# Kernel optimization log

Measured on AMD Instinct MI355X. Metric: run time of the kernel, lower is better.

## Reference

```python
import jax, jax.numpy as jnp
import numpy as np

# --- fixed OpenCV filter kernels ---
# cv2.getGaussianKernel(3, 1): exp(-(i-1)^2/2), normalized -> [0.27407, 0.45186, 0.27407]
_g = np.exp(-((np.arange(3) - 1.0) ** 2) / 2.0)
GAUSS_1D = (_g / _g.sum()).astype(np.float32)
# cv2 Sobel/Laplacian ksize=9 separable parts (unnormalized, as cv2.Laplacian uses):
#   smoothing = binomial row C(8,k); second derivative = C(6,k) conv [1,-2,1]
SMOOTH_9 = np.array([1, 8, 28, 56, 70, 56, 28, 8, 1], dtype=np.float32)
D2_9 = np.array([1, 4, 4, -4, -10, -4, 4, 4, 1], dtype=np.float32)


def _depthwise_conv(x, k2d):
    """Depthwise 2D correlation with BORDER_REFLECT_101 padding (cv2 default).

    x: [N,H,W,C] float, k2d: [kh,kw] float (symmetric, so corr == conv)."""
    C = x.shape[-1]
    rh, rw = k2d.shape[0] // 2, k2d.shape[1] // 2
    # jnp 'reflect' == OpenCV BORDER_REFLECT_101 (edge pixel not duplicated)
    xp = jnp.pad(x, ((0, 0), (rh, rh), (rw, rw), (0, 0)), mode='reflect')
    k = jnp.broadcast_to(k2d[:, :, None, None], (k2d.shape[0], k2d.shape[1], 1, C))
    return jax.lax.conv_general_dilated(
        xp, k, window_strides=(1, 1), padding='VALID',
        dimension_numbers=('NHWC', 'HWIO', 'NHWC'),
        feature_group_count=C)


def setup_inputs() -> dict:
    key = jax.random.key(0)
    # uint8-range image batch, as the original layer feeds uint8 data to OpenCV
    x = jax.random.uniform(key, (32, 512, 512, 3), dtype=jnp.float32) * 255.0
    return {"x": x}


def reference(x) -> jnp.ndarray:
    g = jnp.asarray(GAUSS_1D)
    blur = _depthwise_conv(x, jnp.outer(g, g))  # GaussianBlur(ksize=3, sigma=1)
    lap_k = jnp.asarray(np.outer(SMOOTH_9, D2_9) + np.outer(D2_9, SMOOTH_9))
    lap = _depthwise_conv(blur, lap_k) + 1.0  # delta = 1
    # CV_8UC1 destination depth -> saturate to [0, 255]
    return jnp.clip(lap, 0.0, 255.0)
```

## Files before the change

### kernel.cpp

```cpp
#include <hip/hip_runtime.h>


#define TH 32
#define TW 32
#define FW (TW*3)
#define BW (TW+8)
#define BF (BW*3)
#define BH (TH+8)
#define XHMAX (TH+10)
#define HIMG 512
#define WIMG 512
#define ROWF (WIMG*3)

#define SM_TOTAL 12480

__device__ __forceinline__ int reflect101(int i, int n) {
    i = (i < 0) ? -i : i;
    return (i >= n) ? (2 * n - 2 - i) : i;
}

__device__ __forceinline__ float4 fma4(float s, const float4& a, const float4& b) {
    return make_float4(fmaf(s, a.x, b.x), fmaf(s, a.y, b.y),
                       fmaf(s, a.z, b.z), fmaf(s, a.w, b.w));
}

__global__ __launch_bounds__(256, 3)
void log_fused(const float* __restrict__ x, float* __restrict__ out) {
    __shared__ __align__(16) float smem[SM_TOTAL];
    __shared__ int brow[BH][3];
    float* const blur  = smem;
    float* const hblur = smem + 4800;
    float* const t1    = smem + 4800;
    float* const t2    = smem + 8640;

    const int tid  = threadIdx.x;
    const int col0 = blockIdx.x * TW;
    const int row0 = blockIdx.y * TH;
    const int n    = blockIdx.z;

    const int R0    = max(0, row0 - 5);
    const int R1    = min(HIMG - 1, row0 + TH + 4);
    const int nrows = R1 - R0 + 1;

    if (tid < BH) {
        int gr = reflect101(row0 - 4 + tid, HIMG);
        brow[tid][0] = reflect101(gr - 1, HIMG) - R0;
        brow[tid][1] = gr - R0;
        brow[tid][2] = reflect101(gr + 1, HIMG) - R0;
    }

    const float G0 = 0.2740686190f, G1 = 0.4518627620f;

    if (tid < 240) {
        const int lc  = tid % BF;
        const int rg  = tid / BF;
        const int lcp = lc / 3;
        const int ch  = lc - 3 * lcp;
        const int gc  = reflect101(col0 - 4 + lcp, WIMG);
        const int xm  = reflect101(gc - 1, WIMG) * 3 + ch;
        const int x0  = gc * 3 + ch;
        const int xp  = reflect101(gc + 1, WIMG) * 3 + ch;
        const float* xr = x + ((size_t)n * HIMG + (size_t)(R0 + rg)) * ROWF;
        for (int r = rg; r < nrows; r += 2, xr += 2 * ROWF) {
            hblur[r * BF + lc] = G0 * (xr[xm] + xr[xp]) + G1 * xr[x0];
        }
    }
    __syncthreads();

    for (int e = tid; e < (BH * BF) / 4; e += 256) {
        int lr = e / (BF / 4);
        int qc = e - lr * (BF / 4);
        int lc = qc * 4;
        const float4 a = *(const float4*)&hblur[brow[lr][0] * BF + lc];
        const float4 b = *(const float4*)&hblur[brow[lr][1] * BF + lc];
        const float4 c = *(const float4*)&hblur[brow[lr][2] * BF + lc];
        float4 r;
        r.x = G0 * (a.x + c.x) + G1 * b.x;
        r.y = G0 * (a.y + c.y) + G1 * b.y;
        r.z = G0 * (a.z + c.z) + G1 * b.z;
        r.w = G0 * (a.w + c.w) + G1 * b.w;
        *(float4*)&blur[lr * BF + lc] = r;
    }
    __syncthreads();

    const float S9[9] = {1.f, 8.f, 28.f, 56.f, 70.f, 56.f, 28.f, 8.f, 1.f};
    const float D9[9] = {1.f, 4.f, 4.f, -4.f, -10.f, -4.f, 4.f, 4.f, 1.f};

    for (int g = tid; g < (TH / 2) * (BF / 4); g += 256) {
        int rg  = g / (BF / 4);
        int qc  = g - rg * (BF / 4);
        int lr0 = rg * 2;
        int lc  = qc * 4;
        float4 w[10];
        #pragma unroll
        for (int k = 0; k < 10; ++k)
            w[k] = *(const float4*)&blur[(lr0 + k) * BF + lc];
        float4 a1r0 = make_float4(0.f, 0.f, 0.f, 0.f), a2r0 = a1r0;
        float4 a1r1 = a1r0, a2r1 = a1r0;
        #pragma unroll
        for (int k = 0; k < 9; ++k) {
            a1r0 = fma4(S9[k], w[k],     a1r0);
            a2r0 = fma4(D9[k], w[k],     a2r0);
            a1r1 = fma4(S9[k], w[k + 1], a1r1);
            a2r1 = fma4(D9[k], w[k + 1], a2r1);
        }
        *(float4*)&t1[(lr0    ) * BF + lc] = a1r0;
        *(float4*)&t1[(lr0 + 1) * BF + lc] = a1r1;
        *(float4*)&t2[(lr0    ) * BF + lc] = a2r0;
        *(float4*)&t2[(lr0 + 1) * BF + lc] = a2r1;
    }
    __syncthreads();

    float* const outn = out + (size_t)n * HIMG * ROWF;
    for (int g = tid; g < TH * (FW / 8); g += 256) {
        int lr = g / (FW / 8);
        int qp = g - lr * (FW / 8);
        int lc = qp * 8;
        float w1[32], w2[32];
        #pragma unroll
        for (int q = 0; q < 8; ++q) {
            float4 v = *(const float4*)&t1[lr * BF + lc + 4 * q];
            w1[4*q+0] = v.x; w1[4*q+1] = v.y; w1[4*q+2] = v.z; w1[4*q+3] = v.w;
            float4 u = *(const float4*)&t2[lr * BF + lc + 4 * q];
            w2[4*q+0] = u.x; w2[4*q+1] = u.y; w2[4*q+2] = u.z; w2[4*q+3] = u.w;
        }
        float o[8];
        #pragma unroll
        for (int j = 0; j < 8; ++j) {
            float a = 1.0f;
            #pragma unroll
            for (int k = 0; k < 9; ++k) {
                a = fmaf(D9[k], w1[j + 3 * k], a);
                a = fmaf(S9[k], w2[j + 3 * k], a);
            }
            o[j] = fminf(fmaxf(a, 0.0f), 255.0f);
        }
        float* op = outn + (size_t)(row0 + lr) * ROWF + (size_t)(col0 * 3 + lc);
        *(float4*)&op[0] = make_float4(o[0], o[1], o[2], o[3]);
        *(float4*)&op[4] = make_float4(o[4], o[5], o[6], o[7]);
    }
}

extern "C" void kernel_launch(void* const* d_in, const int* in_sizes, int n_in,
                              void* d_out, int out_size, void* d_ws, size_t ws_size,
                              hipStream_t stream) {
    const float* x = (const float*)d_in[0];
    float* outp = (float*)d_out;
    const int nimg = in_sizes[0] / (HIMG * WIMG * 3);
    dim3 grid(WIMG / TW, HIMG / TH, nimg);
    log_fused<<<grid, dim3(256, 1, 1), 0, stream>>>(x, outp);
}
```

Before: 252.7 us.

## Halve tile height, vectorize interior horizontal blur, and shrink per-thread register windows

Tile height drops from 32 to 16 rows, shared memory shrinks, and launch bounds rise to 6 blocks per CU to raise occupancy. Interior column tiles load the input with float4 reads and compute the horizontal Gaussian from register shuffles, while edge tiles keep the reflected scalar path. The final horizontal pass now produces 4 outputs per thread from a 28-float streaming window instead of 8 outputs from 32-float arrays, which lowers register pressure. The cost is more halo overhead per output (8 halo rows per 16 instead of per 32), which means more redundant input reads and blur work.

```diff
diff --git a/kernel.cpp b/kernel.cpp
--- a/kernel.cpp
+++ b/kernel.cpp
@@ -1,18 +1,16 @@
 #include <hip/hip_runtime.h>
 
 
-#define TH 32
+#define TH 16
 #define TW 32
 #define FW (TW*3)
-#define BW (TW+8)
-#define BF (BW*3)
+#define BF ((TW+8)*3)
 #define BH (TH+8)
-#define XHMAX (TH+10)
 #define HIMG 512
 #define WIMG 512
 #define ROWF (WIMG*3)
 
-#define SM_TOTAL 12480
+#define SM_TOTAL 6720
 
 __device__ __forceinline__ int reflect101(int i, int n) {
     i = (i < 0) ? -i : i;
@@ -24,14 +22,13 @@
                        fmaf(s, a.z, b.z), fmaf(s, a.w, b.w));
 }
 
-__global__ __launch_bounds__(256, 3)
+__global__ __launch_bounds__(256, 6)
 void log_fused(const float* __restrict__ x, float* __restrict__ out) {
     __shared__ __align__(16) float smem[SM_TOTAL];
-    __shared__ int brow[BH][3];
-    float* const blur  = smem;
-    float* const hblur = smem + 4800;
-    float* const t1    = smem + 4800;
-    float* const t2    = smem + 8640;
+    float* const hblur = smem;
+    float* const t1    = smem;
+    float* const t2    = smem + TH * BF;
+    float* const blur  = smem + 2 * TH * BF;
 
     const int tid  = threadIdx.x;
     const int col0 = blockIdx.x * TW;
@@ -42,38 +39,57 @@
     const int R1    = min(HIMG - 1, row0 + TH + 4);
     const int nrows = R1 - R0 + 1;
 
-    if (tid < BH) {
-        int gr = reflect101(row0 - 4 + tid, HIMG);
-        brow[tid][0] = reflect101(gr - 1, HIMG) - R0;
-        brow[tid][1] = gr - R0;
-        brow[tid][2] = reflect101(gr + 1, HIMG) - R0;
-    }
-
     const float G0 = 0.2740686190f, G1 = 0.4518627620f;
 
-    if (tid < 240) {
-        const int lc  = tid % BF;
-        const int rg  = tid / BF;
-        const int lcp = lc / 3;
-        const int ch  = lc - 3 * lcp;
-        const int gc  = reflect101(col0 - 4 + lcp, WIMG);
-        const int xm  = reflect101(gc - 1, WIMG) * 3 + ch;
-        const int x0  = gc * 3 + ch;
-        const int xp  = reflect101(gc + 1, WIMG) * 3 + ch;
-        const float* xr = x + ((size_t)n * HIMG + (size_t)(R0 + rg)) * ROWF;
-        for (int r = rg; r < nrows; r += 2, xr += 2 * ROWF) {
-            hblur[r * BF + lc] = G0 * (xr[xm] + xr[xp]) + G1 * xr[x0];
+    const bool edgecol = (col0 == 0) || (col0 + TW == WIMG);
+    if (!edgecol) {
+        if (tid < 240) {
+            const int cg = tid % 30;
+            const int rg = tid / 30;
+            const float* xb = x + ((size_t)n * HIMG + (size_t)(R0 + rg)) * ROWF
+                                + (3 * (col0 - 4) + 4 * cg - 4);
+            float* hb = hblur + rg * BF + 4 * cg;
+            for (int r = rg; r < nrows; r += 8, xb += 8 * ROWF, hb += 8 * BF) {
+                const float4 a = *(const float4*)(xb);
+                const float4 b = *(const float4*)(xb + 4);
+                const float4 c = *(const float4*)(xb + 8);
+                float4 o;
+                o.x = G0 * (a.y + b.w) + G1 * b.x;
+                o.y = G0 * (a.z + c.x) + G1 * b.y;
+                o.z = G0 * (a.w + c.y) + G1 * b.z;
+                o.w = G0 * (b.x + c.z) + G1 * b.w;
+                *(float4*)hb = o;
+            }
+        }
+    } else {
+        if (tid < 240) {
+            const int lc  = tid % BF;
+            const int rg  = tid / BF;
+            const int lcp = lc / 3;
+            const int ch  = lc - 3 * lcp;
+            const int gc  = reflect101(col0 - 4 + lcp, WIMG);
+            const int xm  = reflect101(gc - 1, WIMG) * 3 + ch;
+            const int x0  = gc * 3 + ch;
+            const int xp  = reflect101(gc + 1, WIMG) * 3 + ch;
+            const float* xr = x + ((size_t)n * HIMG + (size_t)(R0 + rg)) * ROWF;
+            for (int r = rg; r < nrows; r += 2, xr += 2 * ROWF) {
+                hblur[r * BF + lc] = G0 * (xr[xm] + xr[xp]) + G1 * xr[x0];
+            }
         }
     }
     __syncthreads();
 
-    for (int e = tid; e < (BH * BF) / 4; e += 256) {
-        int lr = e / (BF / 4);
-        int qc = e - lr * (BF / 4);
-        int lc = qc * 4;
-        const float4 a = *(const float4*)&hblur[brow[lr][0] * BF + lc];
-        const float4 b = *(const float4*)&hblur[brow[lr][1] * BF + lc];
-        const float4 c = *(const float4*)&hblur[brow[lr][2] * BF + lc];
+    for (int e = tid; e < BH * (BF / 4); e += 256) {
+        const int lr = e % BH;
+        const int qc = e / BH;
+        const int gr = reflect101(row0 - 4 + lr, HIMG);
+        const int rm = reflect101(gr - 1, HIMG) - R0;
+        const int rz = gr - R0;
+        const int rp = reflect101(gr + 1, HIMG) - R0;
+        const int lc = qc * 4;
+        const float4 a = *(const float4*)&hblur[rm * BF + lc];
+        const float4 b = *(const float4*)&hblur[rz * BF + lc];
+        const float4 c = *(const float4*)&hblur[rp * BF + lc];
         float4 r;
         r.x = G0 * (a.x + c.x) + G1 * b.x;
         r.y = G0 * (a.y + c.y) + G1 * b.y;
@@ -86,11 +102,11 @@
     const float S9[9] = {1.f, 8.f, 28.f, 56.f, 70.f, 56.f, 28.f, 8.f, 1.f};
     const float D9[9] = {1.f, 4.f, 4.f, -4.f, -10.f, -4.f, 4.f, 4.f, 1.f};
 
-    for (int g = tid; g < (TH / 2) * (BF / 4); g += 256) {
-        int rg  = g / (BF / 4);
-        int qc  = g - rg * (BF / 4);
-        int lr0 = rg * 2;
-        int lc  = qc * 4;
+    if (tid < 240) {
+        const int rg  = tid & 7;
+        const int qc  = tid >> 3;
+        const int lr0 = rg * 2;
+        const int lc  = qc * 4;
         float4 w[10];
         #pragma unroll
         for (int k = 0; k < 10; ++k)
@@ -112,32 +128,41 @@
     __syncthreads();
 
     float* const outn = out + (size_t)n * HIMG * ROWF;
-    for (int g = tid; g < TH * (FW / 8); g += 256) {
-        int lr = g / (FW / 8);
-        int qp = g - lr * (FW / 8);
-        int lc = qp * 8;
-        float w1[32], w2[32];
+    for (int g = tid; g < TH * (FW / 4); g += 256) {
+        const int lr = g / (FW / 4 / 1 * 1 / 16 * 16 == 0 ? 1 : 24);
+        (void)lr;
+        const int lr2 = g / 24;
+        const int qp  = g - lr2 * 24;
+        const int c0  = qp * 4;
+        const float* t1r = t1 + lr2 * BF + c0;
+        const float* t2r = t2 + lr2 * BF + c0;
+        float acc[4] = {1.0f, 1.0f, 1.0f, 1.0f};
         #pragma unroll
-        for (int q = 0; q < 8; ++q) {
-            float4 v = *(const float4*)&t1[lr * BF + lc + 4 * q];
-            w1[4*q+0] = v.x; w1[4*q+1] = v.y; w1[4*q+2] = v.z; w1[4*q+3] = v.w;
-            float4 u = *(const float4*)&t2[lr * BF + lc + 4 * q];
-            w2[4*q+0] = u.x; w2[4*q+1] = u.y; w2[4*q+2] = u.z; w2[4*q+3] = u.w;
+        for (int i = 0; i < 7; ++i) {
+            const float4 v1 = *(const float4*)(t1r + 4 * i);
+            const float4 v2 = *(const float4*)(t2r + 4 * i);
+            const float f1[4] = {v1.x, v1.y, v1.z, v1.w};
+            const float f2[4] = {v2.x, v2.y, v2.z, v2.w};
+            #pragma unroll
+            for (int m = 0; m < 4; ++m) {
+                const int pos = 4 * i + m;
+                const int j0  = pos % 3;
+                const int k0  = pos / 3;
+                if (k0 <= 8)
+                    acc[j0] = fmaf(D9[k0], f1[m], fmaf(S9[k0], f2[m], acc[j0]));
+                if (j0 == 0 && pos >= 3) {
+                    const int k1 = k0 - 1;
+                    acc[3] = fmaf(D9[k1], f1[m], fmaf(S9[k1], f2[m], acc[3]));
+                }
+            }
         }
-        float o[8];
-        #pragma unroll
-        for (int j = 0; j < 8; ++j) {
-            float a = 1.0f;
-            #pragma unroll
-            for (int k = 0; k < 9; ++k) {
-                a = fmaf(D9[k], w1[j + 3 * k], a);
-                a = fmaf(S9[k], w2[j + 3 * k], a);
-            }
-            o[j] = fminf(fmaxf(a, 0.0f), 255.0f);
-        }
-        float* op = outn + (size_t)(row0 + lr) * ROWF + (size_t)(col0 * 3 + lc);
-        *(float4*)&op[0] = make_float4(o[0], o[1], o[2], o[3]);
-        *(float4*)&op[4] = make_float4(o[4], o[5], o[6], o[7]);
+        float4 o;
+        o.x = fminf(fmaxf(acc[0], 0.0f), 255.0f);
+        o.y = fminf(fmaxf(acc[1], 0.0f), 255.0f);
+        o.z = fminf(fmaxf(acc[2], 0.0f), 255.0f);
+        o.w = fminf(fmaxf(acc[3], 0.0f), 255.0f);
+        float* op = outn + (size_t)(row0 + lr2) * ROWF + (size_t)(col0 * 3 + c0);
+        *(float4*)op = o;
     }
 }
 
```

After: 239.9 us. -5.0%, faster.
